# Optimization experiments

Measured on AMD Instinct MI355X. Metric: run time of the kernel, lower is better.

## Reference

```python
import jax, jax.numpy as jnp
import numpy as np

GROUPS = 32
EPS = 1e-5


def group_norm(x, scale, bias):
    # x: [b, v, t, s, f]; normalize per (b,v,t) sample over (channels_in_group, s)
    b, v, t, s, f = x.shape
    xg = x.reshape(b, v, t, s, GROUPS, f // GROUPS)
    mean = xg.mean(axis=(3, 5), keepdims=True)
    var = xg.var(axis=(3, 5), keepdims=True)
    xn = ((xg - mean) * jax.lax.rsqrt(var + EPS)).reshape(b, v, t, s, f)
    return xn * scale + bias


def nh_conv(x, adjc, W, b):
    # x: [b,v,t,s,f_in]; adjc: [s, k]; W: [k, f_in, f_out]; b: [f_out]
    x_nh = x[:, :, :, adjc, :]                      # [b,v,t,s,k,f_in]
    return jnp.einsum('bvtskf,kfo->bvtso', x_nh, W) + b


def setup_inputs() -> dict:
    key = jax.random.key(0)
    ks = jax.random.split(key, 12)
    B, V, T, S, F_IN, F_OUT, K = 1, 2, 2, 12288, 128, 256, 9
    x = jax.random.normal(ks[0], (B, V, T, S, F_IN), dtype=jnp.float32)
    adjc = jax.random.randint(ks[1], (S, K), 0, S, dtype=jnp.int32)
    gn1_scale = jnp.ones((F_IN,), jnp.float32)
    gn1_bias = jnp.zeros((F_IN,), jnp.float32)
    gn2_scale = jnp.ones((F_OUT,), jnp.float32)
    gn2_bias = jnp.zeros((F_OUT,), jnp.float32)
    W_skip = jax.random.normal(ks[2], (F_IN, F_OUT), jnp.float32) / np.sqrt(F_IN)
    b_skip = jnp.zeros((F_OUT,), jnp.float32)
    W1 = jax.random.normal(ks[3], (K, F_IN, F_OUT), jnp.float32) / np.sqrt(K * F_IN)
    b1 = jnp.zeros((F_OUT,), jnp.float32)
    W2 = jax.random.normal(ks[4], (K, F_OUT, F_OUT), jnp.float32) / np.sqrt(K * F_OUT)
    b2 = jnp.zeros((F_OUT,), jnp.float32)
    return dict(x=x, adjc=adjc, gn1_scale=gn1_scale, gn1_bias=gn1_bias,
                gn2_scale=gn2_scale, gn2_bias=gn2_bias, W_skip=W_skip, b_skip=b_skip,
                W1=W1, b1=b1, W2=W2, b2=b2)


def reference(x, gn1_scale, gn1_bias, gn2_scale, gn2_bias, W_skip, b_skip,
              W1, b1, W2, b2, adjc):
    # skip_layer: ProjLayer with zoom_diff=0 -> plain Linear in->out
    x_res = jnp.einsum('bvtsf,fo->bvtso', x, W_skip) + b_skip
    # norm1 + SiLU (updownconv is Identity when zooms match and in==in feats)
    h = jax.nn.silu(group_norm(x, gn1_scale, gn1_bias))
    # conv1: neighbor-gather linear [k, f_in] -> f_out
    h = nh_conv(h, adjc, W1, b1)
    # emb_layer = Identity; norm2 + SiLU
    h = jax.nn.silu(group_norm(h, gn2_scale, gn2_bias))
    # conv2 + residual
    h = nh_conv(h, adjc, W2, b2)
    return h + x_res
```

## Files before the change

kernel.cpp:

```cpp
#include <hip/hip_runtime.h>
#include <hip/hip_bf16.h>

typedef __bf16 bf16_t;
typedef __bf16 bf16x8 __attribute__((ext_vector_type(8)));
typedef float f32x4 __attribute__((ext_vector_type(4)));

#define S_TOT 12288
#define F_IN 128
#define F_OUT 256
#define EPS 1e-5f

static __device__ __forceinline__ float silu_f(float v) {
  return v / (1.0f + __expf(-v));
}

static __device__ __forceinline__ void gll16(const bf16_t* g, bf16_t* l) {
  __builtin_amdgcn_global_load_lds(
      (const __attribute__((address_space(1))) void*)(const void*)g,
      (__attribute__((address_space(3))) void*)(void*)l, 16, 0, 0);
}

__global__ void pack_weights(const float* __restrict__ W1,
                             const float* __restrict__ W2,
                             const float* __restrict__ Wsk,
                             bf16_t* __restrict__ W1p,
                             bf16_t* __restrict__ W2p,
                             bf16_t* __restrict__ Wsp) {
  int w = blockIdx.x * 4 + (threadIdx.x >> 6);
  int l = threadIdx.x & 63;
  int lo = l & 15, hi = l >> 4;
  const float* src;
  bf16_t* dst;
  int fbase, obase;
  if (w < 576) {
    int k = w >> 6, rem = w & 63, kc = rem >> 4, cb = rem & 15;
    src = W1 + k * 32768;
    dst = W1p + (size_t)w * 512;
    fbase = 32 * kc + 8 * hi; obase = 16 * cb + lo;
  } else if (w < 1728) {
    int idx = w - 576;
    int k = idx >> 7, rem = idx & 127, kc = rem >> 4, cb = rem & 15;
    src = W2 + k * 65536;
    dst = W2p + (size_t)idx * 512;
    fbase = 32 * kc + 8 * hi; obase = 16 * cb + lo;
  } else {
    int idx = w - 1728;
    int kc = idx >> 4, cb = idx & 15;
    src = Wsk;
    dst = Wsp + (size_t)idx * 512;
    fbase = 32 * kc + 8 * hi; obase = 16 * cb + lo;
  }
  bf16x8 v;
#pragma unroll
  for (int j = 0; j < 8; ++j)
    v[j] = (bf16_t)src[(fbase + j) * 256 + obase];
  *(bf16x8*)(dst + l * 8) = v;
}

__global__ void gn1_stats(const float* __restrict__ x,
                          float* __restrict__ sum1, float* __restrict__ ss1) {
  int vt = blockIdx.y;
  int s0 = blockIdx.x * 256;
  int t = threadIdx.x;
  int col = t & 31, ro = t >> 5;
  float s_ = 0.f, q_ = 0.f;
  const f32x4* xp = (const f32x4*)(x + ((size_t)vt * S_TOT + s0) * F_IN);
#pragma unroll 4
  for (int it = 0; it < 32; ++it) {
    f32x4 v = xp[(size_t)(it * 8 + ro) * 32 + col];
    s_ += v[0] + v[1] + v[2] + v[3];
    q_ += v[0]*v[0] + v[1]*v[1] + v[2]*v[2] + v[3]*v[3];
  }
  __shared__ float gs[32], gq[32];
  if (t < 32) { gs[t] = 0.f; gq[t] = 0.f; }
  __syncthreads();
  atomicAdd(&gs[col], s_);
  atomicAdd(&gq[col], q_);
  __syncthreads();
  if (t < 32) {
    atomicAdd(&sum1[vt * 32 + t], gs[t]);
    atomicAdd(&ss1[vt * 32 + t], gq[t]);
  }
}

__global__ void apply_gn1(const float* __restrict__ x,
                          const float* __restrict__ sum1, const float* __restrict__ ss1,
                          const float* __restrict__ gs, const float* __restrict__ gb,
                          bf16_t* __restrict__ h1) {
  size_t base = ((size_t)blockIdx.x * 256 + threadIdx.x) * 8;
  int vt = (int)(base / ((size_t)S_TOT * F_IN));
  int c0 = (int)(base & (F_IN - 1));
  const f32x4* xp = (const f32x4*)(x + base);
  f32x4 v0 = xp[0], v1 = xp[1];
  float N = (float)(S_TOT * 4);
  bf16x8 o;
#pragma unroll
  for (int gi = 0; gi < 2; ++gi) {
    int g = (c0 >> 2) + gi;
    float mean = sum1[vt * 32 + g] / N;
    float var = ss1[vt * 32 + g] / N - mean * mean;
    float r = rsqrtf(var + EPS);
    f32x4 v = gi ? v1 : v0;
#pragma unroll
    for (int j = 0; j < 4; ++j) {
      int c = g * 4 + j;
      float a = r * gs[c];
      float b = gb[c] - mean * a;
      o[gi * 4 + j] = (bf16_t)silu_f(v[j] * a + b);
    }
  }
  *(bf16x8*)(h1 + base) = o;
}

__global__ void apply_gn2(bf16_t* __restrict__ h,
                          const float* __restrict__ sum_c, const float* __restrict__ ss_c,
                          const float* __restrict__ gs, const float* __restrict__ gb) {
  size_t base = ((size_t)blockIdx.x * 256 + threadIdx.x) * 8;
  int vt = (int)(base / ((size_t)S_TOT * F_OUT));
  int c0 = (int)(base & (F_OUT - 1));
  int g = c0 >> 3;
  bf16x8 v = *(const bf16x8*)(h + base);
  float sg = 0.f, qg = 0.f;
#pragma unroll
  for (int j = 0; j < 8; ++j) {
    sg += sum_c[vt * 256 + g * 8 + j];
    qg += ss_c[vt * 256 + g * 8 + j];
  }
  float N = (float)(S_TOT * 8);
  float mean = sg / N;
  float var = qg / N - mean * mean;
  float r = rsqrtf(var + EPS);
  bf16x8 o;
#pragma unroll
  for (int j = 0; j < 8; ++j) {
    int c = g * 8 + j;
    float a = r * gs[c];
    float b = gb[c] - mean * a;
    o[j] = (bf16_t)silu_f((float)v[j] * a + b);
  }
  *(bf16x8*)(h + base) = o;
}

template<int RE, int NSUB, bool XSK>
__global__ __launch_bounds__(256, 4) void conv_kernel(
    const bf16_t* __restrict__ hsrc, const bf16_t* __restrict__ Wp,
    const bf16_t* __restrict__ Wsp, const float* __restrict__ x,
    const int* __restrict__ adjc, const float* __restrict__ bias,
    const float* __restrict__ biask, bf16_t* __restrict__ outb,
    float* __restrict__ outf, float* __restrict__ sum_c, float* __restrict__ ss_c) {
  const int tid = threadIdx.x;
  const int wv = tid >> 6, l = tid & 63;
  const int lo = l & 15, hi = l >> 4;
  const int mw = wv >> 1, nw = wv & 1;

  int swz = ((blockIdx.x & 7) * 96) + (blockIdx.x >> 3);
  int vt = swz / 192;
  int rem = swz - vt * 192;
  int sblk = rem >> 1, nsp = rem & 1;
  int s0 = sblk * 128;

  __shared__ int adjs[1152];
  __shared__ bf16_t ab[2][4096];
  __shared__ bf16_t bb[2][4096];

  for (int i = tid; i < 1152; i += 256) adjs[i] = adjc[s0 * 9 + i];
  __syncthreads();

  const bf16_t* hb = hsrc + (size_t)vt * ((size_t)S_TOT * RE);
  constexpr int TPK = RE / 32;
  constexpr int NMAIN = XSK ? (NSUB - 4) : NSUB;

  auto stageA = [&](int buf, int s) {
    int tap = s / TPK, chunk = s % TPK;
#pragma unroll
    for (int j2 = 0; j2 < 2; ++j2) {
      int j = wv * 2 + j2;
      int row = j * 16 + (l >> 2);
      int segs = (l & 3) ^ ((row >> 1) & 3);
      int arow = adjs[row * 9 + tap];
      const bf16_t* g = hb + (size_t)arow * RE + chunk * 32 + segs * 8;
      gll16(g, &ab[buf][j * 512]);
    }
  };
  auto stageB = [&](int buf, const bf16_t* wsrc, int kcg) {
#pragma unroll
    for (int j2 = 0; j2 < 2; ++j2) {
      int ul = wv * 2 + j2;
      const bf16_t* g = wsrc + ((size_t)(kcg * 16 + nsp * 8 + ul)) * 512 + l * 8;
      gll16(g, &bb[buf][ul * 512]);
    }
  };
  auto stageX = [&](int buf, int sx) {
    int row = tid >> 1, h = tid & 1;
    const float* xr = x + ((size_t)vt * S_TOT + s0 + row) * F_IN + sx * 32 + h * 16;
    f32x4 xv[4];
#pragma unroll
    for (int i = 0; i < 4; ++i) xv[i] = *(const f32x4*)(xr + i * 4);
#pragma unroll
    for (int i = 0; i < 2; ++i) {
      bf16x8 w;
#pragma unroll
      for (int jj = 0; jj < 4; ++jj) {
        w[jj] = (bf16_t)xv[2 * i][jj];
        w[4 + jj] = (bf16_t)xv[2 * i + 1][jj];
      }
      int seg = 2 * h + i;
      *(bf16x8*)(&ab[buf][row * 32 + (((seg ^ ((row >> 1) & 3))) << 3)]) = w;
    }
  };

  f32x4 acc[4][4] = {};
  auto compute = [&](int buf) {
    bf16x8 bfr[4];
#pragma unroll
    for (int ni = 0; ni < 4; ++ni)
      bfr[ni] = *(const bf16x8*)(&bb[buf][(nw * 4 + ni) * 512 + l * 8]);
    bf16x8 afr[4];
#pragma unroll
    for (int mi = 0; mi < 4; ++mi) {
      int rr = mw * 64 + mi * 16 + lo;
      afr[mi] = *(const bf16x8*)(&ab[buf][rr * 32 + ((hi ^ ((rr >> 1) & 3)) << 3)]);
    }
#pragma unroll
    for (int mi = 0; mi < 4; ++mi)
#pragma unroll
      for (int ni = 0; ni < 4; ++ni)
        acc[mi][ni] = __builtin_amdgcn_mfma_f32_16x16x32_bf16(afr[mi], bfr[ni], acc[mi][ni], 0, 0, 0);
  };

  stageA(0, 0);
  stageB(0, Wp, 0);
  __syncthreads();

  for (int s = 0; s < NSUB; ++s) {
    int buf = s & 1;
    int s1 = s + 1;
    if (s1 < NMAIN) {
      stageA(buf ^ 1, s1);
      stageB(buf ^ 1, Wp, s1);
    } else if (XSK && s1 < NSUB) {
      int sx = s1 - NMAIN;
      stageX(buf ^ 1, sx);
      stageB(buf ^ 1, Wsp, sx);
    }
    compute(buf);
    __syncthreads();
  }

  if (!XSK) {
    bf16_t* ob = outb + ((size_t)vt * S_TOT + s0) * 256;
#pragma unroll
    for (int ni = 0; ni < 4; ++ni) {
      int o = nsp * 128 + nw * 64 + ni * 16 + lo;
      float bv = bias[o];
      float s_ = 0.f, q_ = 0.f;
#pragma unroll
      for (int mi = 0; mi < 4; ++mi)
#pragma unroll
        for (int r2 = 0; r2 < 4; ++r2) {
          int srow = mw * 64 + mi * 16 + hi * 4 + r2;
          float v = acc[mi][ni][r2] + bv;
          ob[(size_t)srow * 256 + o] = (bf16_t)v;
          s_ += v; q_ += v * v;
        }
      s_ += __shfl_xor(s_, 16); s_ += __shfl_xor(s_, 32);
      q_ += __shfl_xor(q_, 16); q_ += __shfl_xor(q_, 32);
      if (hi == 0) {
        atomicAdd(&sum_c[vt * 256 + o], s_);
        atomicAdd(&ss_c[vt * 256 + o], q_);
      }
    }
  } else {
    float* of = outf + ((size_t)vt * S_TOT + s0) * 256;
#pragma unroll
    for (int ni = 0; ni < 4; ++ni) {
      int o = nsp * 128 + nw * 64 + ni * 16 + lo;
      float bv = bias[o] + biask[o];
#pragma unroll
      for (int mi = 0; mi < 4; ++mi)
#pragma unroll
        for (int r2 = 0; r2 < 4; ++r2) {
          int srow = mw * 64 + mi * 16 + hi * 4 + r2;
          of[(size_t)srow * 256 + o] = acc[mi][ni][r2] + bv;
        }
    }
  }
}

extern "C" void kernel_launch(void* const* d_in, const int* in_sizes, int n_in,
                              void* d_out, int out_size, void* d_ws, size_t ws_size,
                              hipStream_t stream) {
  const float* x      = (const float*)d_in[0];
  const int*   adjc   = (const int*)d_in[1];
  const float* gn1_s  = (const float*)d_in[2];
  const float* gn1_b  = (const float*)d_in[3];
  const float* gn2_s  = (const float*)d_in[4];
  const float* gn2_b  = (const float*)d_in[5];
  const float* W_skip = (const float*)d_in[6];
  const float* b_skip = (const float*)d_in[7];
  const float* W1     = (const float*)d_in[8];
  const float* b1     = (const float*)d_in[9];
  const float* W2     = (const float*)d_in[10];
  const float* b2     = (const float*)d_in[11];
  float* out = (float*)d_out;

  float* sum1  = (float*)d_ws;
  float* ss1   = sum1 + 128;
  float* sum_c = ss1 + 128;
  float* ss_c  = sum_c + 1024;
  float* a1    = ss_c + 1024;
  float* b1a   = a1 + 512;
  float* a2    = b1a + 512;
  float* b2a   = a2 + 1024;
  bf16_t* W1p  = (bf16_t*)(b2a + 1024);
  bf16_t* W2p  = W1p + 294912;
  bf16_t* Wsp  = W2p + 589824;
  bf16_t* h1   = Wsp + 32768;
  bf16_t* out1 = h1 + 6291456;

  hipMemsetAsync(sum1, 0, (128 + 128 + 1024 + 1024) * sizeof(float), stream);
  pack_weights<<<448, 256, 0, stream>>>(W1, W2, W_skip, W1p, W2p, Wsp);
  gn1_stats<<<dim3(48, 4), 256, 0, stream>>>(x, sum1, ss1);
  apply_gn1<<<3072, 256, 0, stream>>>(x, sum1, ss1, gn1_s, gn1_b, h1);
  conv_kernel<128, 36, false><<<768, 256, 0, stream>>>(
      h1, W1p, nullptr, nullptr, adjc, b1, nullptr, out1, nullptr, sum_c, ss_c);
  apply_gn2<<<6144, 256, 0, stream>>>(out1, sum_c, ss_c, gn2_s, gn2_b);
  conv_kernel<256, 76, true><<<768, 256, 0, stream>>>(
      out1, W2p, Wsp, x, adjc, b2, b_skip, nullptr, out, nullptr, nullptr);
}
```

Baseline: 154.1 us.

## Triple-buffer conv LDS staging with vmcnt waits and MFMA priority boost

```diff
diff --git a/kernel.cpp b/kernel.cpp
--- a/kernel.cpp
+++ b/kernel.cpp
@@ -142,7 +142,7 @@
 }
 
 template<int RE, int NSUB, bool XSK>
-__global__ __launch_bounds__(256, 4) void conv_kernel(
+__global__ __launch_bounds__(256, 3) void conv_kernel(
     const bf16_t* __restrict__ hsrc, const bf16_t* __restrict__ Wp,
     const bf16_t* __restrict__ Wsp, const float* __restrict__ x,
     const int* __restrict__ adjc, const float* __restrict__ bias,
@@ -160,8 +160,8 @@
   int s0 = sblk * 128;
 
   __shared__ int adjs[1152];
-  __shared__ bf16_t ab[2][4096];
-  __shared__ bf16_t bb[2][4096];
+  __shared__ bf16_t ab[3][4096];
+  __shared__ bf16_t bb[3][4096];
 
   for (int i = tid; i < 1152; i += 256) adjs[i] = adjc[s0 * 9 + i];
   __syncthreads();
@@ -221,30 +221,40 @@
       int rr = mw * 64 + mi * 16 + lo;
       afr[mi] = *(const bf16x8*)(&ab[buf][rr * 32 + ((hi ^ ((rr >> 1) & 3)) << 3)]);
     }
+    __builtin_amdgcn_s_setprio(1);
 #pragma unroll
     for (int mi = 0; mi < 4; ++mi)
 #pragma unroll
       for (int ni = 0; ni < 4; ++ni)
         acc[mi][ni] = __builtin_amdgcn_mfma_f32_16x16x32_bf16(afr[mi], bfr[ni], acc[mi][ni], 0, 0, 0);
+    __builtin_amdgcn_s_setprio(0);
   };
 
-  stageA(0, 0);
-  stageB(0, Wp, 0);
-  __syncthreads();
-
-  for (int s = 0; s < NSUB; ++s) {
-    int buf = s & 1;
-    int s1 = s + 1;
-    if (s1 < NMAIN) {
-      stageA(buf ^ 1, s1);
-      stageB(buf ^ 1, Wp, s1);
-    } else if (XSK && s1 < NSUB) {
-      int sx = s1 - NMAIN;
-      stageX(buf ^ 1, sx);
-      stageB(buf ^ 1, Wsp, sx);
-    }
-    compute(buf);
-    __syncthreads();
+  stageA(0, 0); stageB(0, Wp, 0);
+  stageA(1, 1); stageB(1, Wp, 1);
+  for (int s = 0; s < NMAIN; ++s) {
+    if (s + 1 < NMAIN) asm volatile("s_waitcnt vmcnt(4)" ::: "memory");
+    else               asm volatile("s_waitcnt vmcnt(0)" ::: "memory");
+    __builtin_amdgcn_s_barrier();
+    __builtin_amdgcn_sched_barrier(0);
+    int s2 = s + 2;
+    if (s2 < NMAIN) {
+      int nb = s2 % 3;
+      stageA(nb, s2);
+      stageB(nb, Wp, s2);
+    }
+    compute(s % 3);
+  }
+
+  if (XSK) {
+    for (int sx = 0; sx < 4; ++sx) {
+      int cur = (NMAIN + sx) % 3;
+      __syncthreads();
+      stageX(cur, sx);
+      stageB(cur, Wsp, sx);
+      __syncthreads();
+      compute(cur);
+    }
   }
 
   if (!XSK) {
@@ -308,11 +318,8 @@
   float* ss1   = sum1 + 128;
   float* sum_c = ss1 + 128;
   float* ss_c  = sum_c + 1024;
-  float* a1    = ss_c + 1024;
-  float* b1a   = a1 + 512;
-  float* a2    = b1a + 512;
-  float* b2a   = a2 + 1024;
-  bf16_t* W1p  = (bf16_t*)(b2a + 1024);
+  float* pad   = ss_c + 1024;
+  bf16_t* W1p  = (bf16_t*)(pad + 3072);
   bf16_t* W2p  = W1p + 294912;
   bf16_t* Wsp  = W2p + 589824;
   bf16_t* h1   = Wsp + 32768;
```

New measurement: 153.2 us. About the same (-0.6%).
